# Kernel optimization log

Hardware: AMD Instinct MI355X
Metric: run time of the kernel (lower is better)

## Reference

```python
import jax, jax.numpy as jnp
import numpy as np
from jax import lax

N_STATES = 4096
N_OBS = 512
SEQ_LEN = 8192


def setup_inputs() -> dict:
    key = jax.random.key(0)
    k1, k2, k3 = jax.random.split(key, 3)
    observations = jax.random.randint(k1, (SEQ_LEN,), 0, N_OBS, dtype=jnp.int32)
    # row-stochastic transition matrix (single action, as in TorchCHMMSensory)
    T = jax.random.uniform(k2, (N_STATES, N_STATES), dtype=jnp.float32) + 1e-10
    T = T / T.sum(axis=1, keepdims=True)
    Pi_x = jax.random.uniform(k3, (N_STATES,), dtype=jnp.float32) + 1e-10
    Pi_x = Pi_x / Pi_x.sum()
    return {"T": T, "Pi_x": Pi_x, "observations": observations, "n_observations": N_OBS}


def _forward_backward(T, Pi_x, observations, n_observations):
    """Scaled CHMM forward-backward. Clone-structured deterministic emission:
    state s emits observation s // n_clones, so emission is an indicator mask."""
    S = T.shape[0]
    n_clones = S // n_observations
    state_obs = jnp.arange(S, dtype=jnp.int32) // n_clones  # [S]
    mask = (state_obs[None, :] == observations[:, None]).astype(T.dtype)  # [L, S]

    # --- forward pass (scaled alphas) ---
    a0 = Pi_x * mask[0]
    c0 = a0.sum()
    a0 = a0 / c0

    def fwd_step(alpha, m):
        a = (alpha @ T) * m   # message passing + clone-block restriction
        c = a.sum()
        a = a / c
        return a, (a, c)

    _, (al, cs) = lax.scan(fwd_step, a0, mask[1:])
    alphas = jnp.concatenate([a0[None], al])          # [L, S]
    cs = jnp.concatenate([c0[None], cs])              # [L]
    log_lik = jnp.sum(jnp.log(cs))

    # --- backward pass (scaled betas) ---
    def bwd_step(beta, mc):
        m, c = mc
        b = (T @ (m * beta)) / c
        return b, b

    bL = jnp.ones((S,), dtype=T.dtype)
    _, betas_rev = lax.scan(bwd_step, bL, (mask[1:], cs[1:]), reverse=True)
    betas = jnp.concatenate([betas_rev, bL[None]])    # [L, S]

    gamma = alphas * betas
    gamma = gamma / gamma.sum(axis=1, keepdims=True)  # posteriors [L, S]
    return log_lik, gamma


def reference(T, Pi_x, observations, n_observations):
    return _forward_backward(T, Pi_x, observations, n_observations)
```

## Files before the change

### kernel.cpp

```cpp
#include <hip/hip_runtime.h>


#define NSTATES 4096
#define NBLK    8
#define LSEQ    8192
#define NSTEPS  8191
#define CHK     32
#define NCH     256
#define NGRP    16
#define GSZ     16

#define OFF_P   0u
#define OFF_G2  16384u
#define OFF_LLP 17408u
#define FLG_F1  17664u
#define FLG_F2  17920u
#define FLG_F3  17936u
#define MAGIC   0x5A17C0DEu

__device__ __forceinline__ float aload(float* p) {
    return __hip_atomic_load(p, __ATOMIC_RELAXED, __HIP_MEMORY_SCOPE_AGENT);
}
__device__ __forceinline__ void astore(float* p, float v) {
    __hip_atomic_store(p, v, __ATOMIC_RELAXED, __HIP_MEMORY_SCOPE_AGENT);
}
__device__ __forceinline__ unsigned aloadu(unsigned* p) {
    return __hip_atomic_load(p, __ATOMIC_RELAXED, __HIP_MEMORY_SCOPE_AGENT);
}
__device__ __forceinline__ void astoreu(unsigned* p, unsigned v) {
    __hip_atomic_store(p, v, __ATOMIC_RELAXED, __HIP_MEMORY_SCOPE_AGENT);
}
#define VMFENCE()  asm volatile("s_waitcnt vmcnt(0)" ::: "memory")
#define LDSFENCE() asm volatile("s_waitcnt lgkmcnt(0)" ::: "memory")

__device__ __forceinline__ int expof(float x) {
    return (int)((__float_as_uint(x) >> 23) & 0xff) - 127;
}

__global__ __launch_bounds__(256) void kFB(const float* __restrict__ T,
                                           const float* __restrict__ Pi,
                                           const int* __restrict__ obs,
                                           float* __restrict__ out,
                                           float* __restrict__ ws)
{
    __shared__ float sM[CHK * 64];
    __shared__ float sDuty[GSZ * 64];
    __shared__ float sG2[NGRP * 64];
    __shared__ float sGP[GSZ * 64];
    __shared__ float sA[(CHK + 1) * 8];
    __shared__ float sB[(CHK + 1) * 8];
    __shared__ float sGv[CHK * 8];
    __shared__ int   sObs[CHK + 1];
    unsigned* flg = reinterpret_cast<unsigned*>(ws);
    const int tid = threadIdx.x;
    const int blk = blockIdx.x;

    if (blk >= NCH) {
        const int c = blk - NCH;
        const int r0 = c * CHK;
        if (tid < CHK + 1) {
            int t = r0 - 1 + tid;
            sObs[tid] = (t >= 0) ? obs[t] : 0;
        }
        __syncthreads();
        float4* o4 = reinterpret_cast<float4*>(out);
        const float4 z = make_float4(0.f, 0.f, 0.f, 0.f);
        const int wv = tid >> 6, lane = tid & 63;
        int w2r[8];
#pragma unroll
        for (int k = 0; k < 8; ++k) w2r[k] = sObs[1 + wv * 8 + k] * 2;
#pragma unroll
        for (int k = 0; k < 8; ++k) {
            const int rr = wv * 8 + k;
            float4* rowp = o4 + (size_t)(r0 + rr) * 1024;
            const int w2 = w2r[k];
#pragma unroll
            for (int s = 0; s < 16; ++s) {
                int pos = s * 64 + lane;
                if (pos != 0 && (unsigned)(pos - w2) > 2u) rowp[pos] = z;
            }
        }
        {
            const int rr = tid >> 3, role = tid & 7;
            const int r = r0 + rr;
            const int ob = sObs[1 + rr];
            const int obPrev = sObs[rr];
            const int m = r * 1024 + ob * 2;
            const int ks = r * 1024;
            const bool fullStraddle = (r != 0) && (obPrev != 511) && (ob != 0);
            if (role == 0) {
                if (fullStraddle) o4[ks] = z;
                else if (r != 0 && obPrev != 511) out[(size_t)4 * ks] = 0.f;
            } else if (role <= 3) {
                if (!fullStraddle && ob != 0) out[(size_t)4 * ks + role] = 0.f;
            } else if (role <= 6) {
                if (ob <= 510) out[(size_t)4 * m + 9 + (role - 4)] = 0.f;
            } else {
                if (ob >= 1) out[(size_t)4 * m] = 0.f;
            }
            if (tid == 255 && c == NCH - 1 && sObs[CHK] != 511)
                out[(size_t)LSEQ * NSTATES] = 0.f;
        }
        return;
    }

    if (tid >= 64) return;
    __builtin_amdgcn_s_setprio(1);
    const int b = blk;
    const int g = b >> 4, rIn = b & 15;
    const int t0 = b * CHK;
    const int n = min(CHK, NSTEPS - t0);
    float ll0 = 0.f;
    int kTot = 0;
    const int i = tid >> 3, j = tid & 7;

#pragma unroll
    for (int w = 0; w < 4; ++w) {
        int u = tid + 64 * w;
        int dt = u >> 3, ri = u & 7;
        if (dt < n) {
            int t = t0 + dt;
            int row = obs[t] * NBLK + ri;
            int col = obs[t + 1] * NBLK;
            const float4* src = reinterpret_cast<const float4*>(T + (size_t)row * NSTATES + col);
            float4 v0 = src[0], v1 = src[1];
            float vv[8] = {v0.x, v0.y, v0.z, v0.w, v1.x, v1.y, v1.z, v1.w};
            float* base = &sM[dt * 64 + ri];
#pragma unroll
            for (int jj = 0; jj < 8; ++jj) base[jj * 8] = vv[jj];
        }
    }
    if (tid < CHK) sObs[tid] = obs[t0 + tid];
    LDSFENCE();

    {
        float p = sM[j * 8 + i];
        float m[8], mn[8];
#pragma unroll
        for (int k = 0; k < 8; ++k) m[k] = sM[64 + j * 8 + k];
        for (int dt = 1; dt < n; ++dt) {
            int dtn = min(dt + 1, n - 1);
#pragma unroll
            for (int k = 0; k < 8; ++k) mn[k] = sM[dtn * 64 + j * 8 + k];
            float pn = 0.f;
#pragma unroll
            for (int k = 0; k < 8; ++k) pn = fmaf(__shfl(p, i * 8 + k, 64), m[k], pn);
            if ((dt & 3) == 0) {
                int ke = expof(__shfl(pn, 0, 64));
                pn = ldexpf(pn, -ke);
                kTot += ke;
            }
            p = pn;
#pragma unroll
            for (int k = 0; k < 8; ++k) m[k] = mn[k];
        }
        {
            int ke = expof(__shfl(p, 0, 64));
            p = ldexpf(p, -ke);
            kTot += ke;
        }
        astore(&ws[OFF_P + b * 64 + j * 8 + i], p);
    }
    VMFENCE();
    if (tid == 0) astoreu(&flg[FLG_F1 + b], MAGIC);

    if (b < NGRP) {
        for (;;) {
            bool ok = true;
            if (tid < GSZ)
                ok = aloadu(&flg[FLG_F1 + GSZ * b + tid]) == MAGIC;
            if (__all(ok)) break;
            __builtin_amdgcn_s_sleep(1);
        }
        {
            float rb[16];
#pragma unroll
            for (int k = 0; k < 16; ++k)
                rb[k] = aload(&ws[OFF_P + (size_t)b * GSZ * 64 + k * 64 + tid]);
#pragma unroll
            for (int k = 0; k < 16; ++k) sDuty[k * 64 + tid] = rb[k];
        }
        LDSFENCE();
        float p = sDuty[j * 8 + i];
        float m[8], mn[8];
#pragma unroll
        for (int k = 0; k < 8; ++k) m[k] = sDuty[64 + j * 8 + k];
        for (int r = 1; r < GSZ; ++r) {
            int rn = min(r + 1, GSZ - 1);
#pragma unroll
            for (int k = 0; k < 8; ++k) mn[k] = sDuty[rn * 64 + j * 8 + k];
            float pn = 0.f;
#pragma unroll
            for (int k = 0; k < 8; ++k) pn = fmaf(__shfl(p, i * 8 + k, 64), m[k], pn);
            if ((r & 1) == 0 || r == GSZ - 1) {
                int ke = expof(__shfl(pn, 0, 64));
                pn = ldexpf(pn, -ke);
            }
            p = pn;
#pragma unroll
            for (int k = 0; k < 8; ++k) m[k] = mn[k];
        }
        astore(&ws[OFF_G2 + b * 64 + j * 8 + i], p);
        VMFENCE();
        if (tid == 0) astoreu(&flg[FLG_F2 + b], MAGIC);
    }

    for (;;) {
        bool ok = true;
        if (tid < NGRP)
            ok = aloadu(&flg[FLG_F2 + tid]) == MAGIC;
        if (__all(ok)) break;
        __builtin_amdgcn_s_sleep(1);
    }
    {
        float ra[16], rb[16];
#pragma unroll
        for (int k = 0; k < 16; ++k) ra[k] = aload(&ws[OFF_G2 + k * 64 + tid]);
#pragma unroll
        for (int k = 0; k < 16; ++k)
            rb[k] = aload(&ws[OFF_P + (size_t)g * GSZ * 64 + k * 64 + tid]);
#pragma unroll
        for (int k = 0; k < 16; ++k) sG2[k * 64 + tid] = ra[k];
#pragma unroll
        for (int k = 0; k < 16; ++k) sGP[k * 64 + tid] = rb[k];
    }
    LDSFENCE();

    if (tid < 16) {
        const int grp = tid >> 3, l8 = tid & 7;
        const int st = grp ? 8 : 1;
        const int boff = grp ? l8 : l8 * 8;
        float v[8], vb[8];
        {
            float a = Pi[obs[0] * NBLK + l8];
            float s0 = a;
            s0 += __shfl_xor(s0, 1); s0 += __shfl_xor(s0, 2); s0 += __shfl_xor(s0, 4);
            float rs0 = 1.0f / s0;
#pragma unroll
            for (int q = 0; q < 8; ++q) v[q] = grp ? 0.125f : __shfl(a, q, 8) * rs0;
            ll0 = __logf(s0);
        }
        const int cap = grp ? (NGRP - 1 - g) : g;
        if (cap == 0) {
#pragma unroll
            for (int q = 0; q < 8; ++q) vb[q] = v[q];
        }
        {
            float m[8], mn[8];
            int gi0 = grp ? (NGRP - 1) : 0;
#pragma unroll
            for (int q = 0; q < 8; ++q) m[q] = sG2[gi0 * 64 + boff + q * st];
            for (int r = 0; r < NGRP - 1; ++r) {
                int rp = min(r + 1, NGRP - 2);
                int gin = grp ? (NGRP - 1 - rp) : rp;
#pragma unroll
                for (int q = 0; q < 8; ++q) mn[q] = sG2[gin * 64 + boff + q * st];
                float u = 0.f;
#pragma unroll
                for (int q = 0; q < 8; ++q) u = fmaf(v[q], m[q], u);
                float s = 0.f;
#pragma unroll
                for (int q = 0; q < 8; ++q) { float x = __shfl(u, q, 8); v[q] = x; s += x; }
                float rs = 1.0f / s;
#pragma unroll
                for (int q = 0; q < 8; ++q) v[q] *= rs;
                if (r + 1 == cap) {
#pragma unroll
                    for (int q = 0; q < 8; ++q) vb[q] = v[q];
                }
#pragma unroll
                for (int q = 0; q < 8; ++q) m[q] = mn[q];
            }
        }
#pragma unroll
        for (int q = 0; q < 8; ++q) v[q] = vb[q];
        const int cnt = grp ? (GSZ - 1 - rIn) : rIn;
        {
            float m[8], mn[8];
            int lc0 = grp ? (GSZ - 1) : 0;
#pragma unroll
            for (int k = 0; k < 8; ++k) m[k] = sGP[lc0 * 64 + boff + k * st];
            for (int q = 0; q < GSZ - 1; ++q) {
                bool act = q < cnt;
                int qn = q + 1 < cnt ? q + 1 : 0;
                int lcn = grp ? (GSZ - 1 - qn) : qn;
#pragma unroll
                for (int k = 0; k < 8; ++k) mn[k] = sGP[lcn * 64 + boff + k * st];
                float u = 0.f;
#pragma unroll
                for (int k = 0; k < 8; ++k) u = fmaf(v[k], m[k], u);
                float s = 0.f;
                float vn[8];
#pragma unroll
                for (int k = 0; k < 8; ++k) { float x = __shfl(u, k, 8); vn[k] = x; s += x; }
                float rs = 1.0f / s;
#pragma unroll
                for (int k = 0; k < 8; ++k) v[k] = act ? vn[k] * rs : v[k];
#pragma unroll
                for (int k = 0; k < 8; ++k) m[k] = mn[k];
            }
        }
        if (grp == 0) {
            float u = 0.f;
#pragma unroll
            for (int q2 = 0; q2 < 8; ++q2)
                u = fmaf(v[q2], sGP[rIn * 64 + l8 * 8 + q2], u);
            float ssum = u;
            ssum += __shfl_xor(ssum, 1); ssum += __shfl_xor(ssum, 2); ssum += __shfl_xor(ssum, 4);
            if (l8 == 0)
                astore(&ws[OFF_LLP + b], __logf(ssum) + (float)kTot * 0.69314718055994531f);
        }
        float* hist = grp ? sB : sA;
        hist[(grp ? n : 0) * 8 + l8] = v[l8];
        int mt0 = grp ? (n - 1) : 0;
        float m[8], mn[8];
#pragma unroll
        for (int q = 0; q < 8; ++q) m[q] = sM[mt0 * 64 + boff + q * st];
        for (int rr = 0; rr < n; ++rr) {
            int rn2 = min(rr + 1, n - 1);
            int mtn = grp ? (n - 1 - rn2) : rn2;
#pragma unroll
            for (int q = 0; q < 8; ++q) mn[q] = sM[mtn * 64 + boff + q * st];
            float u = 0.f;
#pragma unroll
            for (int q = 0; q < 8; ++q) u = fmaf(v[q], m[q], u);
            float s = 0.f;
#pragma unroll
            for (int q = 0; q < 8; ++q) { float x = __shfl(u, q, 8); v[q] = x; s += x; }
            float rs = 1.0f / s;
#pragma unroll
            for (int q = 0; q < 8; ++q) v[q] *= rs;
            hist[(grp ? (n - 1 - rr) : (rr + 1)) * 8 + l8] = v[l8];
#pragma unroll
            for (int q = 0; q < 8; ++q) m[q] = mn[q];
        }
    }
    LDSFENCE();

    {
        const int r0l = tid >> 3, ii = tid & 7;
#pragma unroll
        for (int k = 0; k < 4; ++k) {
            int rr = r0l + k * 8;
            float gp = sA[rr * 8 + ii] * sB[rr * 8 + ii];
            float gs = gp;
            gs += __shfl_xor(gs, 1); gs += __shfl_xor(gs, 2); gs += __shfl_xor(gs, 4);
            sGv[rr * 8 + ii] = gp / gs;
        }
    }
    LDSFENCE();
    VMFENCE();
    if (tid == 0) astoreu(&flg[FLG_F3 + b], MAGIC);
    __builtin_amdgcn_s_setprio(0);

    if (tid < CHK) {
        const int r = t0 + tid;
        const int ob = sObs[tid];
        const size_t W = (size_t)r * NSTATES + ob * NBLK;
        const float* gv = &sGv[tid * 8];
        out[W + 1] = gv[0];
        out[W + 2] = gv[1];
        out[W + 3] = gv[2];
        reinterpret_cast<float4*>(out)[W / 4 + 1] = make_float4(gv[3], gv[4], gv[5], gv[6]);
        out[W + 8] = gv[7];
    }

    if (b == 0) {
        for (;;) {
            bool ok = true;
#pragma unroll
            for (int q = 0; q < 4; ++q)
                ok = ok && (aloadu(&flg[FLG_F3 + tid * 4 + q]) == MAGIC);
            if (__all(ok)) break;
            __builtin_amdgcn_s_sleep(1);
        }
        float part = 0.f;
#pragma unroll
        for (int q = 0; q < 4; ++q) part += aload(&ws[OFF_LLP + tid * 4 + q]);
        part += __shfl_xor(part, 32); part += __shfl_xor(part, 16);
        part += __shfl_xor(part, 8);  part += __shfl_xor(part, 4);
        part += __shfl_xor(part, 2);  part += __shfl_xor(part, 1);
        if (tid == 0) out[0] = part + ll0;
    }
}

extern "C" void kernel_launch(void* const* d_in, const int* in_sizes, int n_in,
                              void* d_out, int out_size, void* d_ws, size_t ws_size,
                              hipStream_t stream)
{
    const float* T   = (const float*)d_in[0];
    const float* Pi  = (const float*)d_in[1];
    const int*   obs = (const int*)d_in[2];
    float* out = (float*)d_out;
    float* ws  = (float*)d_ws;

    kFB<<<NCH * 2, 256, 0, stream>>>(T, Pi, obs, out, ws);
}
```

Baseline: 41.53 us.

## Merge zero-fill blocks into compute blocks using idle waves

Launches half as many blocks and has waves 1-3 of each compute block zero-fill the output rows of that chunk, which the separate zero-fill blocks used to do while those waves simply exited. Wave 0 handles the boundary zero stores after its compute. This removes the extra blocks and puts the bandwidth-bound fill next to the latency-bound chain, at the cost of the fill sharing a CU with the critical wave and possibly slowing it down.

Result: slower. 42.90 us (+3.3%).

```diff
diff --git a/kernel.cpp b/kernel.cpp
--- a/kernel.cpp
+++ b/kernel.cpp
@@ -50,41 +50,310 @@
     __shared__ float sA[(CHK + 1) * 8];
     __shared__ float sB[(CHK + 1) * 8];
     __shared__ float sGv[CHK * 8];
-    __shared__ int   sObs[CHK + 1];
+    __shared__ int   sO2[CHK + 1];
     unsigned* flg = reinterpret_cast<unsigned*>(ws);
     const int tid = threadIdx.x;
-    const int blk = blockIdx.x;
-
-    if (blk >= NCH) {
-        const int c = blk - NCH;
-        const int r0 = c * CHK;
-        if (tid < CHK + 1) {
-            int t = r0 - 1 + tid;
-            sObs[tid] = (t >= 0) ? obs[t] : 0;
-        }
-        __syncthreads();
+    const int b = blockIdx.x;
+    const int t0 = b * CHK;
+
+    if (tid >= 64) {
+        const int w = tid >> 6;
+        const int lane = tid & 63;
         float4* o4 = reinterpret_cast<float4*>(out);
         const float4 z = make_float4(0.f, 0.f, 0.f, 0.f);
-        const int wv = tid >> 6, lane = tid & 63;
-        int w2r[8];
-#pragma unroll
-        for (int k = 0; k < 8; ++k) w2r[k] = sObs[1 + wv * 8 + k] * 2;
-#pragma unroll
-        for (int k = 0; k < 8; ++k) {
-            const int rr = wv * 8 + k;
-            float4* rowp = o4 + (size_t)(r0 + rr) * 1024;
-            const int w2 = w2r[k];
-#pragma unroll
-            for (int s = 0; s < 16; ++s) {
-                int pos = s * 64 + lane;
-                if (pos != 0 && (unsigned)(pos - w2) > 2u) rowp[pos] = z;
-            }
+        int obr[11];
+#pragma unroll
+        for (int k = 0; k < 11; ++k) {
+            int rr = 3 * k + (w - 1);
+            obr[k] = (rr < CHK) ? obs[t0 + rr] : 0;
+        }
+#pragma unroll
+        for (int k = 0; k < 11; ++k) {
+            int rr = 3 * k + (w - 1);
+            if (rr < CHK) {
+                const int w2 = obr[k] * 2;
+                float4* rowp = o4 + (size_t)(t0 + rr) * 1024;
+#pragma unroll
+                for (int s = 0; s < 16; ++s) {
+                    int pos = s * 64 + lane;
+                    if (pos != 0 && (unsigned)(pos - w2) > 2u) rowp[pos] = z;
+                }
+            }
+        }
+        return;
+    }
+
+    __builtin_amdgcn_s_setprio(1);
+    const int g = b >> 4, rIn = b & 15;
+    const int n = min(CHK, NSTEPS - t0);
+    float ll0 = 0.f;
+    int kTot = 0;
+    const int i = tid >> 3, j = tid & 7;
+
+#pragma unroll
+    for (int w = 0; w < 4; ++w) {
+        int u = tid + 64 * w;
+        int dt = u >> 3, ri = u & 7;
+        if (dt < n) {
+            int t = t0 + dt;
+            int row = obs[t] * NBLK + ri;
+            int col = obs[t + 1] * NBLK;
+            const float4* src = reinterpret_cast<const float4*>(T + (size_t)row * NSTATES + col);
+            float4 v0 = src[0], v1 = src[1];
+            float vv[8] = {v0.x, v0.y, v0.z, v0.w, v1.x, v1.y, v1.z, v1.w};
+            float* base = &sM[dt * 64 + ri];
+#pragma unroll
+            for (int jj = 0; jj < 8; ++jj) base[jj * 8] = vv[jj];
+        }
+    }
+    if (tid < CHK + 1) {
+        int t = t0 - 1 + tid;
+        sO2[tid] = (t >= 0) ? obs[t] : 0;
+    }
+    LDSFENCE();
+
+    {
+        float p = sM[j * 8 + i];
+        float m[8], mn[8];
+#pragma unroll
+        for (int k = 0; k < 8; ++k) m[k] = sM[64 + j * 8 + k];
+        for (int dt = 1; dt < n; ++dt) {
+            int dtn = min(dt + 1, n - 1);
+#pragma unroll
+            for (int k = 0; k < 8; ++k) mn[k] = sM[dtn * 64 + j * 8 + k];
+            float pn = 0.f;
+#pragma unroll
+            for (int k = 0; k < 8; ++k) pn = fmaf(__shfl(p, i * 8 + k, 64), m[k], pn);
+            if ((dt & 3) == 0) {
+                int ke = expof(__shfl(pn, 0, 64));
+                pn = ldexpf(pn, -ke);
+                kTot += ke;
+            }
+            p = pn;
+#pragma unroll
+            for (int k = 0; k < 8; ++k) m[k] = mn[k];
         }
         {
-            const int rr = tid >> 3, role = tid & 7;
-            const int r = r0 + rr;
-            const int ob = sObs[1 + rr];
-            const int obPrev = sObs[rr];
+            int ke = expof(__shfl(p, 0, 64));
+            p = ldexpf(p, -ke);
+            kTot += ke;
+        }
+        astore(&ws[OFF_P + b * 64 + j * 8 + i], p);
+    }
+    VMFENCE();
+    if (tid == 0) astoreu(&flg[FLG_F1 + b], MAGIC);
+
+    if (b < NGRP) {
+        for (;;) {
+            bool ok = true;
+            if (tid < GSZ)
+                ok = aloadu(&flg[FLG_F1 + GSZ * b + tid]) == MAGIC;
+            if (__all(ok)) break;
+            __builtin_amdgcn_s_sleep(1);
+        }
+        {
+            float rb[16];
+#pragma unroll
+            for (int k = 0; k < 16; ++k)
+                rb[k] = aload(&ws[OFF_P + (size_t)b * GSZ * 64 + k * 64 + tid]);
+#pragma unroll
+            for (int k = 0; k < 16; ++k) sDuty[k * 64 + tid] = rb[k];
+        }
+        LDSFENCE();
+        float p = sDuty[j * 8 + i];
+        float m[8], mn[8];
+#pragma unroll
+        for (int k = 0; k < 8; ++k) m[k] = sDuty[64 + j * 8 + k];
+        for (int r = 1; r < GSZ; ++r) {
+            int rn = min(r + 1, GSZ - 1);
+#pragma unroll
+            for (int k = 0; k < 8; ++k) mn[k] = sDuty[rn * 64 + j * 8 + k];
+            float pn = 0.f;
+#pragma unroll
+            for (int k = 0; k < 8; ++k) pn = fmaf(__shfl(p, i * 8 + k, 64), m[k], pn);
+            if ((r & 1) == 0 || r == GSZ - 1) {
+                int ke = expof(__shfl(pn, 0, 64));
+                pn = ldexpf(pn, -ke);
+            }
+            p = pn;
+#pragma unroll
+            for (int k = 0; k < 8; ++k) m[k] = mn[k];
+        }
+        astore(&ws[OFF_G2 + b * 64 + j * 8 + i], p);
+        VMFENCE();
+        if (tid == 0) astoreu(&flg[FLG_F2 + b], MAGIC);
+    }
+
+    for (;;) {
+        bool ok = true;
+        if (tid < NGRP)
+            ok = aloadu(&flg[FLG_F2 + tid]) == MAGIC;
+        if (__all(ok)) break;
+        __builtin_amdgcn_s_sleep(1);
+    }
+    {
+        float ra[16], rb[16];
+#pragma unroll
+        for (int k = 0; k < 16; ++k) ra[k] = aload(&ws[OFF_G2 + k * 64 + tid]);
+#pragma unroll
+        for (int k = 0; k < 16; ++k)
+            rb[k] = aload(&ws[OFF_P + (size_t)g * GSZ * 64 + k * 64 + tid]);
+#pragma unroll
+        for (int k = 0; k < 16; ++k) sG2[k * 64 + tid] = ra[k];
+#pragma unroll
+        for (int k = 0; k < 16; ++k) sGP[k * 64 + tid] = rb[k];
+    }
+    LDSFENCE();
+
+    if (tid < 16) {
+        const int grp = tid >> 3, l8 = tid & 7;
+        const int st = grp ? 8 : 1;
+        const int boff = grp ? l8 : l8 * 8;
+        float v[8], vb[8];
+        {
+            float a = Pi[obs[0] * NBLK + l8];
+            float s0 = a;
+            s0 += __shfl_xor(s0, 1); s0 += __shfl_xor(s0, 2); s0 += __shfl_xor(s0, 4);
+            float rs0 = 1.0f / s0;
+#pragma unroll
+            for (int q = 0; q < 8; ++q) v[q] = grp ? 0.125f : __shfl(a, q, 8) * rs0;
+            ll0 = __logf(s0);
+        }
+        const int cap = grp ? (NGRP - 1 - g) : g;
+        if (cap == 0) {
+#pragma unroll
+            for (int q = 0; q < 8; ++q) vb[q] = v[q];
+        }
+        {
+            float m[8], mn[8];
+            int gi0 = grp ? (NGRP - 1) : 0;
+#pragma unroll
+            for (int q = 0; q < 8; ++q) m[q] = sG2[gi0 * 64 + boff + q * st];
+            for (int r = 0; r < NGRP - 1; ++r) {
+                int rp = min(r + 1, NGRP - 2);
+                int gin = grp ? (NGRP - 1 - rp) : rp;
+#pragma unroll
+                for (int q = 0; q < 8; ++q) mn[q] = sG2[gin * 64 + boff + q * st];
+                float u = 0.f;
+#pragma unroll
+                for (int q = 0; q < 8; ++q) u = fmaf(v[q], m[q], u);
+                float s = 0.f;
+#pragma unroll
+                for (int q = 0; q < 8; ++q) { float x = __shfl(u, q, 8); v[q] = x; s += x; }
+                float rs = 1.0f / s;
+#pragma unroll
+                for (int q = 0; q < 8; ++q) v[q] *= rs;
+                if (r + 1 == cap) {
+#pragma unroll
+                    for (int q = 0; q < 8; ++q) vb[q] = v[q];
+                }
+#pragma unroll
+                for (int q = 0; q < 8; ++q) m[q] = mn[q];
+            }
+        }
+#pragma unroll
+        for (int q = 0; q < 8; ++q) v[q] = vb[q];
+        const int cnt = grp ? (GSZ - 1 - rIn) : rIn;
+        {
+            float m[8], mn[8];
+            int lc0 = grp ? (GSZ - 1) : 0;
+#pragma unroll
+            for (int k = 0; k < 8; ++k) m[k] = sGP[lc0 * 64 + boff + k * st];
+            for (int q = 0; q < GSZ - 1; ++q) {
+                bool act = q < cnt;
+                int qn = q + 1 < cnt ? q + 1 : 0;
+                int lcn = grp ? (GSZ - 1 - qn) : qn;
+#pragma unroll
+                for (int k = 0; k < 8; ++k) mn[k] = sGP[lcn * 64 + boff + k * st];
+                float u = 0.f;
+#pragma unroll
+                for (int k = 0; k < 8; ++k) u = fmaf(v[k], m[k], u);
+                float s = 0.f;
+                float vn[8];
+#pragma unroll
+                for (int k = 0; k < 8; ++k) { float x = __shfl(u, k, 8); vn[k] = x; s += x; }
+                float rs = 1.0f / s;
+#pragma unroll
+                for (int k = 0; k < 8; ++k) v[k] = act ? vn[k] * rs : v[k];
+#pragma unroll
+                for (int k = 0; k < 8; ++k) m[k] = mn[k];
+            }
+        }
+        if (grp == 0) {
+            float u = 0.f;
+#pragma unroll
+            for (int q2 = 0; q2 < 8; ++q2)
+                u = fmaf(v[q2], sGP[rIn * 64 + l8 * 8 + q2], u);
+            float ssum = u;
+            ssum += __shfl_xor(ssum, 1); ssum += __shfl_xor(ssum, 2); ssum += __shfl_xor(ssum, 4);
+            if (l8 == 0)
+                astore(&ws[OFF_LLP + b], __logf(ssum) + (float)kTot * 0.69314718055994531f);
+        }
+        float* hist = grp ? sB : sA;
+        hist[(grp ? n : 0) * 8 + l8] = v[l8];
+        int mt0 = grp ? (n - 1) : 0;
+        float m[8], mn[8];
+#pragma unroll
+        for (int q = 0; q < 8; ++q) m[q] = sM[mt0 * 64 + boff + q * st];
+        for (int rr = 0; rr < n; ++rr) {
+            int rn2 = min(rr + 1, n - 1);
+            int mtn = grp ? (n - 1 - rn2) : rn2;
+#pragma unroll
+            for (int q = 0; q < 8; ++q) mn[q] = sM[mtn * 64 + boff + q * st];
+            float u = 0.f;
+#pragma unroll
+            for (int q = 0; q < 8; ++q) u = fmaf(v[q], m[q], u);
+            float s = 0.f;
+#pragma unroll
+            for (int q = 0; q < 8; ++q) { float x = __shfl(u, q, 8); v[q] = x; s += x; }
+            float rs = 1.0f / s;
+#pragma unroll
+            for (int q = 0; q < 8; ++q) v[q] *= rs;
+            hist[(grp ? (n - 1 - rr) : (rr + 1)) * 8 + l8] = v[l8];
+#pragma unroll
+            for (int q = 0; q < 8; ++q) m[q] = mn[q];
+        }
+    }
+    LDSFENCE();
+
+    {
+        const int r0l = tid >> 3, ii = tid & 7;
+#pragma unroll
+        for (int k = 0; k < 4; ++k) {
+            int rr = r0l + k * 8;
+            float gp = sA[rr * 8 + ii] * sB[rr * 8 + ii];
+            float gs = gp;
+            gs += __shfl_xor(gs, 1); gs += __shfl_xor(gs, 2); gs += __shfl_xor(gs, 4);
+            sGv[rr * 8 + ii] = gp / gs;
+        }
+    }
+    LDSFENCE();
+    VMFENCE();
+    if (tid == 0) astoreu(&flg[FLG_F3 + b], MAGIC);
+    __builtin_amdgcn_s_setprio(0);
+
+    if (tid < CHK) {
+        const int r = t0 + tid;
+        const int ob = sO2[1 + tid];
+        const size_t W = (size_t)r * NSTATES + ob * NBLK;
+        const float* gv = &sGv[tid * 8];
+        out[W + 1] = gv[0];
+        out[W + 2] = gv[1];
+        out[W + 3] = gv[2];
+        reinterpret_cast<float4*>(out)[W / 4 + 1] = make_float4(gv[3], gv[4], gv[5], gv[6]);
+        out[W + 8] = gv[7];
+    }
+
+    {
+        float4* o4 = reinterpret_cast<float4*>(out);
+        const float4 z = make_float4(0.f, 0.f, 0.f, 0.f);
+#pragma unroll
+        for (int it = 0; it < 4; ++it) {
+            const int slot = it * 64 + tid;
+            const int rr = slot >> 3, role = slot & 7;
+            const int r = t0 + rr;
+            const int ob = sO2[1 + rr];
+            const int obPrev = sO2[rr];
             const int m = r * 1024 + ob * 2;
             const int ks = r * 1024;
             const bool fullStraddle = (r != 0) && (obPrev != 511) && (ob != 0);
@@ -98,271 +367,9 @@
             } else {
                 if (ob >= 1) out[(size_t)4 * m] = 0.f;
             }
-            if (tid == 255 && c == NCH - 1 && sObs[CHK] != 511)
-                out[(size_t)LSEQ * NSTATES] = 0.f;
-        }
-        return;
-    }
-
-    if (tid >= 64) return;
-    __builtin_amdgcn_s_setprio(1);
-    const int b = blk;
-    const int g = b >> 4, rIn = b & 15;
-    const int t0 = b * CHK;
-    const int n = min(CHK, NSTEPS - t0);
-    float ll0 = 0.f;
-    int kTot = 0;
-    const int i = tid >> 3, j = tid & 7;
-
-#pragma unroll
-    for (int w = 0; w < 4; ++w) {
-        int u = tid + 64 * w;
-        int dt = u >> 3, ri = u & 7;
-        if (dt < n) {
-            int t = t0 + dt;
-            int row = obs[t] * NBLK + ri;
-            int col = obs[t + 1] * NBLK;
-            const float4* src = reinterpret_cast<const float4*>(T + (size_t)row * NSTATES + col);
-            float4 v0 = src[0], v1 = src[1];
-            float vv[8] = {v0.x, v0.y, v0.z, v0.w, v1.x, v1.y, v1.z, v1.w};
-            float* base = &sM[dt * 64 + ri];
-#pragma unroll
-            for (int jj = 0; jj < 8; ++jj) base[jj * 8] = vv[jj];
-        }
-    }
-    if (tid < CHK) sObs[tid] = obs[t0 + tid];
-    LDSFENCE();
-
-    {
-        float p = sM[j * 8 + i];
-        float m[8], mn[8];
-#pragma unroll
-        for (int k = 0; k < 8; ++k) m[k] = sM[64 + j * 8 + k];
-        for (int dt = 1; dt < n; ++dt) {
-            int dtn = min(dt + 1, n - 1);
-#pragma unroll
-            for (int k = 0; k < 8; ++k) mn[k] = sM[dtn * 64 + j * 8 + k];
-            float pn = 0.f;
-#pragma unroll
-            for (int k = 0; k < 8; ++k) pn = fmaf(__shfl(p, i * 8 + k, 64), m[k], pn);
-            if ((dt & 3) == 0) {
-                int ke = expof(__shfl(pn, 0, 64));
-                pn = ldexpf(pn, -ke);
-                kTot += ke;
-            }
-            p = pn;
-#pragma unroll
-            for (int k = 0; k < 8; ++k) m[k] = mn[k];
-        }
-        {
-            int ke = expof(__shfl(p, 0, 64));
-            p = ldexpf(p, -ke);
-            kTot += ke;
-        }
-        astore(&ws[OFF_P + b * 64 + j * 8 + i], p);
-    }
-    VMFENCE();
-    if (tid == 0) astoreu(&flg[FLG_F1 + b], MAGIC);
-
-    if (b < NGRP) {
-        for (;;) {
-            bool ok = true;
-            if (tid < GSZ)
-                ok = aloadu(&flg[FLG_F1 + GSZ * b + tid]) == MAGIC;
-            if (__all(ok)) break;
-            __builtin_amdgcn_s_sleep(1);
-        }
-        {
-            float rb[16];
-#pragma unroll
-            for (int k = 0; k < 16; ++k)
-                rb[k] = aload(&ws[OFF_P + (size_t)b * GSZ * 64 + k * 64 + tid]);
-#pragma unroll
-            for (int k = 0; k < 16; ++k) sDuty[k * 64 + tid] = rb[k];
-        }
-        LDSFENCE();
-        float p = sDuty[j * 8 + i];
-        float m[8], mn[8];
-#pragma unroll
-        for (int k = 0; k < 8; ++k) m[k] = sDuty[64 + j * 8 + k];
-        for (int r = 1; r < GSZ; ++r) {
-            int rn = min(r + 1, GSZ - 1);
-#pragma unroll
-            for (int k = 0; k < 8; ++k) mn[k] = sDuty[rn * 64 + j * 8 + k];
-            float pn = 0.f;
-#pragma unroll
-            for (int k = 0; k < 8; ++k) pn = fmaf(__shfl(p, i * 8 + k, 64), m[k], pn);
-            if ((r & 1) == 0 || r == GSZ - 1) {
-                int ke = expof(__shfl(pn, 0, 64));
-                pn = ldexpf(pn, -ke);
-            }
-            p = pn;
-#pragma unroll
-            for (int k = 0; k < 8; ++k) m[k] = mn[k];
-        }
-        astore(&ws[OFF_G2 + b * 64 + j * 8 + i], p);
-        VMFENCE();
-        if (tid == 0) astoreu(&flg[FLG_F2 + b], MAGIC);
-    }
-
-    for (;;) {
-        bool ok = true;
-        if (tid < NGRP)
-            ok = aloadu(&flg[FLG_F2 + tid]) == MAGIC;
-        if (__all(ok)) break;
-        __builtin_amdgcn_s_sleep(1);
-    }
-    {
-        float ra[16], rb[16];
-#pragma unroll
-        for (int k = 0; k < 16; ++k) ra[k] = aload(&ws[OFF_G2 + k * 64 + tid]);
-#pragma unroll
-        for (int k = 0; k < 16; ++k)
-            rb[k] = aload(&ws[OFF_P + (size_t)g * GSZ * 64 + k * 64 + tid]);
-#pragma unroll
-        for (int k = 0; k < 16; ++k) sG2[k * 64 + tid] = ra[k];
-#pragma unroll
-        for (int k = 0; k < 16; ++k) sGP[k * 64 + tid] = rb[k];
-    }
-    LDSFENCE();
-
-    if (tid < 16) {
-        const int grp = tid >> 3, l8 = tid & 7;
-        const int st = grp ? 8 : 1;
-        const int boff = grp ? l8 : l8 * 8;
-        float v[8], vb[8];
-        {
-            float a = Pi[obs[0] * NBLK + l8];
-            float s0 = a;
-            s0 += __shfl_xor(s0, 1); s0 += __shfl_xor(s0, 2); s0 += __shfl_xor(s0, 4);
-            float rs0 = 1.0f / s0;
-#pragma unroll
-            for (int q = 0; q < 8; ++q) v[q] = grp ? 0.125f : __shfl(a, q, 8) * rs0;
-            ll0 = __logf(s0);
-        }
-        const int cap = grp ? (NGRP - 1 - g) : g;
-        if (cap == 0) {
-#pragma unroll
-            for (int q = 0; q < 8; ++q) vb[q] = v[q];
-        }
-        {
-            float m[8], mn[8];
-            int gi0 = grp ? (NGRP - 1) : 0;
-#pragma unroll
-            for (int q = 0; q < 8; ++q) m[q] = sG2[gi0 * 64 + boff + q * st];
-            for (int r = 0; r < NGRP - 1; ++r) {
-                int rp = min(r + 1, NGRP - 2);
-                int gin = grp ? (NGRP - 1 - rp) : rp;
-#pragma unroll
-                for (int q = 0; q < 8; ++q) mn[q] = sG2[gin * 64 + boff + q * st];
-                float u = 0.f;
-#pragma unroll
-                for (int q = 0; q < 8; ++q) u = fmaf(v[q], m[q], u);
-                float s = 0.f;
-#pragma unroll
-                for (int q = 0; q < 8; ++q) { float x = __shfl(u, q, 8); v[q] = x; s += x; }
-                float rs = 1.0f / s;
-#pragma unroll
-                for (int q = 0; q < 8; ++q) v[q] *= rs;
-                if (r + 1 == cap) {
-#pragma unroll
-                    for (int q = 0; q < 8; ++q) vb[q] = v[q];
-                }
-#pragma unroll
-                for (int q = 0; q < 8; ++q) m[q] = mn[q];
-            }
-        }
-#pragma unroll
-        for (int q = 0; q < 8; ++q) v[q] = vb[q];
-        const int cnt = grp ? (GSZ - 1 - rIn) : rIn;
-        {
-            float m[8], mn[8];
-            int lc0 = grp ? (GSZ - 1) : 0;
-#pragma unroll
-            for (int k = 0; k < 8; ++k) m[k] = sGP[lc0 * 64 + boff + k * st];
-            for (int q = 0; q < GSZ - 1; ++q) {
-                bool act = q < cnt;
-                int qn = q + 1 < cnt ? q + 1 : 0;
-                int lcn = grp ? (GSZ - 1 - qn) : qn;
-#pragma unroll
-                for (int k = 0; k < 8; ++k) mn[k] = sGP[lcn * 64 + boff + k * st];
-                float u = 0.f;
-#pragma unroll
-                for (int k = 0; k < 8; ++k) u = fmaf(v[k], m[k], u);
-                float s = 0.f;
-                float vn[8];
-#pragma unroll
-                for (int k = 0; k < 8; ++k) { float x = __shfl(u, k, 8); vn[k] = x; s += x; }
-                float rs = 1.0f / s;
-#pragma unroll
-                for (int k = 0; k < 8; ++k) v[k] = act ? vn[k] * rs : v[k];
-#pragma unroll
-                for (int k = 0; k < 8; ++k) m[k] = mn[k];
-            }
-        }
-        if (grp == 0) {
-            float u = 0.f;
-#pragma unroll
-            for (int q2 = 0; q2 < 8; ++q2)
-                u = fmaf(v[q2], sGP[rIn * 64 + l8 * 8 + q2], u);
-            float ssum = u;
-            ssum += __shfl_xor(ssum, 1); ssum += __shfl_xor(ssum, 2); ssum += __shfl_xor(ssum, 4);
-            if (l8 == 0)
-                astore(&ws[OFF_LLP + b], __logf(ssum) + (float)kTot * 0.69314718055994531f);
-        }
-        float* hist = grp ? sB : sA;
-        hist[(grp ? n : 0) * 8 + l8] = v[l8];
-        int mt0 = grp ? (n - 1) : 0;
-        float m[8], mn[8];
-#pragma unroll
-        for (int q = 0; q < 8; ++q) m[q] = sM[mt0 * 64 + boff + q * st];
-        for (int rr = 0; rr < n; ++rr) {
-            int rn2 = min(rr + 1, n - 1);
-            int mtn = grp ? (n - 1 - rn2) : rn2;
-#pragma unroll
-            for (int q = 0; q < 8; ++q) mn[q] = sM[mtn * 64 + boff + q * st];
-            float u = 0.f;
-#pragma unroll
-            for (int q = 0; q < 8; ++q) u = fmaf(v[q], m[q], u);
-            float s = 0.f;
-#pragma unroll
-            for (int q = 0; q < 8; ++q) { float x = __shfl(u, q, 8); v[q] = x; s += x; }
-            float rs = 1.0f / s;
-#pragma unroll
-            for (int q = 0; q < 8; ++q) v[q] *= rs;
-            hist[(grp ? (n - 1 - rr) : (rr + 1)) * 8 + l8] = v[l8];
-#pragma unroll
-            for (int q = 0; q < 8; ++q) m[q] = mn[q];
-        }
-    }
-    LDSFENCE();
-
-    {
-        const int r0l = tid >> 3, ii = tid & 7;
-#pragma unroll
-        for (int k = 0; k < 4; ++k) {
-            int rr = r0l + k * 8;
-            float gp = sA[rr * 8 + ii] * sB[rr * 8 + ii];
-            float gs = gp;
-            gs += __shfl_xor(gs, 1); gs += __shfl_xor(gs, 2); gs += __shfl_xor(gs, 4);
-            sGv[rr * 8 + ii] = gp / gs;
-        }
-    }
-    LDSFENCE();
-    VMFENCE();
-    if (tid == 0) astoreu(&flg[FLG_F3 + b], MAGIC);
-    __builtin_amdgcn_s_setprio(0);
-
-    if (tid < CHK) {
-        const int r = t0 + tid;
-        const int ob = sObs[tid];
-        const size_t W = (size_t)r * NSTATES + ob * NBLK;
-        const float* gv = &sGv[tid * 8];
-        out[W + 1] = gv[0];
-        out[W + 2] = gv[1];
-        out[W + 3] = gv[2];
-        reinterpret_cast<float4*>(out)[W / 4 + 1] = make_float4(gv[3], gv[4], gv[5], gv[6]);
-        out[W + 8] = gv[7];
+        }
+        if (b == NCH - 1 && tid == 0 && sO2[CHK] != 511)
+            out[(size_t)LSEQ * NSTATES] = 0.f;
     }
 
     if (b == 0) {
@@ -394,5 +401,5 @@
     float* out = (float*)d_out;
     float* ws  = (float*)d_ws;
 
-    kFB<<<NCH * 2, 256, 0, stream>>>(T, Pi, obs, out, ws);
-}
+    kFB<<<NCH, 256, 0, stream>>>(T, Pi, obs, out, ws);
+}
```
